# Performance work log

Hardware: AMD Instinct MI355X
Metric: run time of the kernel (lower is better)

Reference implementation:

```python
import jax, jax.numpy as jnp
import numpy as np

BCE_COEFF = 0.2
N_BOXES = 4194304


def setup_inputs() -> dict:
    key = jax.random.key(0)
    k1, k2, k3, k4, k5, k6, k7 = jax.random.split(key, 7)
    n = N_BOXES
    preds = jax.random.normal(k1, (n, 5), dtype=jnp.float32)
    # Build well-formed target boxes (x1<x2, y1<y2) with min size 0.1 in [0,1]
    x1 = jax.random.uniform(k2, (n,), dtype=jnp.float32) * 0.5
    y1 = jax.random.uniform(k3, (n,), dtype=jnp.float32) * 0.5
    w = 0.1 + 0.4 * jax.random.uniform(k4, (n,), dtype=jnp.float32)
    h = 0.1 + 0.4 * jax.random.uniform(k5, (n,), dtype=jnp.float32)
    lbl = jax.random.uniform(k6, (n,), dtype=jnp.float32)  # BCE targets in [0,1]
    target = jnp.stack([lbl, x1, y1, x1 + w, y1 + h], axis=1)
    return {"preds": preds, "target": target}


def _eiou_loss(p, t):
    # p, t: [n, 4] boxes (x1, y1, x2, y2); p already sigmoided
    pred_area = jnp.abs(p[:, 2] - p[:, 0]) * jnp.abs(p[:, 3] - p[:, 1])
    target_area = (t[:, 2] - t[:, 0]) * (t[:, 3] - t[:, 1])
    x_p1 = jnp.minimum(p[:, 2], p[:, 0])
    x_p2 = jnp.maximum(p[:, 2], p[:, 0])
    y_p1 = jnp.minimum(p[:, 1], p[:, 3])
    y_p2 = jnp.maximum(p[:, 1], p[:, 3])
    x1 = jnp.maximum(x_p1, t[:, 0])
    x2 = jnp.minimum(x_p2, t[:, 2])
    y1 = jnp.maximum(y_p1, t[:, 1])
    y2 = jnp.minimum(y_p2, t[:, 3])
    overlap = (x2 - x1) * (y2 - y1)
    overlap = jnp.where(overlap < 0, 0.0, overlap)  # faithful: clamp product only
    x1_c = jnp.minimum(x_p1, t[:, 0])
    x2_c = jnp.maximum(x_p2, t[:, 2])
    y1_c = jnp.minimum(y_p1, t[:, 1])
    y2_c = jnp.maximum(y_p2, t[:, 3])
    c_w = x2_c - x1_c
    c_h = y2_c - y1_c
    w = x_p2 - x_p1
    w_t = t[:, 2] - t[:, 0]
    h = y_p2 - y_p1
    h_t = t[:, 3] - t[:, 1]
    iou = overlap / (target_area + pred_area - overlap)
    cpx = (x_p2 + x_p1) * 0.5
    cpy = (y_p2 + y_p1) * 0.5
    ctx = (t[:, 2] + t[:, 0]) * 0.5
    cty = (t[:, 3] + t[:, 1]) * 0.5
    diag = c_w ** 2 + c_h ** 2
    center_part = ((cpx - ctx) ** 2 + (cpy - cty) ** 2) / diag
    width_part = (w - w_t) ** 2 / c_w ** 2
    height_part = (h - h_t) ** 2 / h_t ** 2  # faithful: h_t**2 denominator
    return 1.0 - (iou - (center_part + width_part + height_part))


def reference(preds, target):
    p_box = jax.nn.sigmoid(preds[:, 1:5])
    eiou = jnp.mean(_eiou_loss(p_box, target[:, 1:5]))
    # binary_cross_entropy_with_logits, mean reduction (numerically stable)
    x = preds[:, 0]
    y = target[:, 0]
    bce = jnp.mean(jnp.maximum(x, 0.0) - x * y + jnp.log1p(jnp.exp(-jnp.abs(x))))
    return BCE_COEFF * bce + eiou
```

## Files before the change

kernel.cpp:

```cpp
#include <hip/hip_runtime.h>

#define N_BOXES 4194304
#define BCE_COEFF 0.2f
#define BLOCK 256
#define WAVES 4
#define WCHUNK 128
#define F4_IN (WCHUNK * 5 / 4)
#define F4_TOT (F4_IN * 2)
#define NBLOCKS 1024
#define BOXES_PER_WAVE (N_BOXES / NBLOCKS / WAVES)
#define ROUNDS (BOXES_PER_WAVE / WCHUNK)

__device__ __forceinline__ void g2lds16(const float4* g, float4* l) {
    __builtin_amdgcn_global_load_lds(
        (const __attribute__((address_space(1))) void*)g,
        (__attribute__((address_space(3))) void*)l,
        16, 0, 0);
}

__global__ __launch_bounds__(BLOCK) void eiou_main(
        const float* __restrict__ preds,
        const float* __restrict__ target,
        float* __restrict__ slots) {
    __shared__ float4 sbuf[WAVES][2][F4_TOT];

    const int t    = threadIdx.x;
    const int lane = t & 63;
    const int w    = t >> 6;
    const float4* const p4 = reinterpret_cast<const float4*>(preds);
    const float4* const t4 = reinterpret_cast<const float4*>(target);

    const size_t wbase = (size_t)blockIdx.x * (N_BOXES / NBLOCKS * 5 / 4)
                       + (size_t)w * (BOXES_PER_WAVE * 5 / 4);

    auto stage = [&](int c, int b) {
        const size_t fb = wbase + (size_t)c * F4_IN;
#pragma unroll
        for (int k = 0; k < 5; ++k) {
            const int q = k * 64 + lane;
            const float4* src = (q < F4_IN) ? (p4 + fb + q)
                                            : (t4 + fb + (q - F4_IN));
            g2lds16(src, &sbuf[w][b][q]);
        }
    };

    stage(0, 0);
    float acc = 0.0f;

    for (int c = 0; c < ROUNDS; ++c) {
        const int b = c & 1;
        if (c + 1 < ROUNDS) {
            asm volatile("s_waitcnt lgkmcnt(0)" ::: "memory");
            stage(c + 1, b ^ 1);
            asm volatile("s_waitcnt vmcnt(5)" ::: "memory");
        } else {
            asm volatile("s_waitcnt vmcnt(0)" ::: "memory");
        }

        const float* __restrict__ s = reinterpret_cast<const float*>(&sbuf[w][b][0]);
#pragma unroll
        for (int j = 0; j < 2; ++j) {
            const int box = lane + j * 64;
            const float* __restrict__ P = s + box * 5;
            const float* __restrict__ T = s + WCHUNK * 5 + box * 5;

            const float x = P[0];
            const float y = T[0];
            const float p0 = __fdividef(1.0f, 1.0f + __expf(-P[1]));
            const float p1 = __fdividef(1.0f, 1.0f + __expf(-P[2]));
            const float p2 = __fdividef(1.0f, 1.0f + __expf(-P[3]));
            const float p3 = __fdividef(1.0f, 1.0f + __expf(-P[4]));
            const float t0 = T[1], t1 = T[2], t2 = T[3], t3 = T[4];

            const float pred_area   = fabsf(p2 - p0) * fabsf(p3 - p1);
            const float target_area = (t2 - t0) * (t3 - t1);

            const float xp1 = fminf(p2, p0), xp2 = fmaxf(p2, p0);
            const float yp1 = fminf(p1, p3), yp2 = fmaxf(p1, p3);

            const float x1 = fmaxf(xp1, t0), x2 = fminf(xp2, t2);
            const float y1 = fmaxf(yp1, t1), y2 = fminf(yp2, t3);

            float ov = (x2 - x1) * (y2 - y1);
            ov = (ov < 0.0f) ? 0.0f : ov;

            const float x1c = fminf(xp1, t0), x2c = fmaxf(xp2, t2);
            const float y1c = fminf(yp1, t1), y2c = fmaxf(yp2, t3);

            const float cw = x2c - x1c, ch = y2c - y1c;
            const float w2 = xp2 - xp1, wt = t2 - t0;
            const float h  = yp2 - yp1, ht = t3 - t1;

            const float iou = __fdividef(ov, target_area + pred_area - ov);

            const float cpx = (xp2 + xp1) * 0.5f, cpy = (yp2 + yp1) * 0.5f;
            const float ctx = (t2 + t0) * 0.5f,   cty = (t3 + t1) * 0.5f;
            const float diag = cw * cw + ch * ch;
            const float dx = cpx - ctx, dy = cpy - cty;

            const float center_part = __fdividef(dx * dx + dy * dy, diag);
            const float dwv = w2 - wt;
            const float width_part  = __fdividef(dwv * dwv, cw * cw);
            const float dhv = h - ht;
            const float height_part = __fdividef(dhv * dhv, ht * ht);

            const float eiou = 1.0f - (iou - (center_part + width_part + height_part));

            const float bce = fmaxf(x, 0.0f) - x * y
                            + __logf(1.0f + __expf(-fabsf(x)));

            acc += BCE_COEFF * bce + eiou;
        }
    }

#pragma unroll
    for (int off = 32; off > 0; off >>= 1)
        acc += __shfl_down(acc, off);

    __syncthreads();
    float* sf = reinterpret_cast<float*>(&sbuf[0][0][0]);
    if (lane == 0) sf[w] = acc;
    __syncthreads();
    if (t == 0) slots[blockIdx.x] = (sf[0] + sf[1]) + (sf[2] + sf[3]);
}

__global__ __launch_bounds__(256) void reduce_slots_kernel(
        const float* __restrict__ slots,
        float* __restrict__ out) {
    const float4 v4 = reinterpret_cast<const float4*>(slots)[threadIdx.x];
    float v = (v4.x + v4.y) + (v4.z + v4.w);
#pragma unroll
    for (int off = 32; off > 0; off >>= 1)
        v += __shfl_down(v, off);

    __shared__ float ws[4];
    const int lane = threadIdx.x & 63;
    const int wid  = threadIdx.x >> 6;
    if (lane == 0) ws[wid] = v;
    __syncthreads();
    if (threadIdx.x == 0)
        out[0] = ((ws[0] + ws[1]) + (ws[2] + ws[3])) * (1.0f / (float)N_BOXES);
}

extern "C" void kernel_launch(void* const* d_in, const int* in_sizes, int n_in,
                              void* d_out, int out_size, void* d_ws, size_t ws_size,
                              hipStream_t stream) {
    const float* preds  = (const float*)d_in[0];
    const float* target = (const float*)d_in[1];
    float* slots = (float*)d_ws;
    float* out   = (float*)d_out;

    eiou_main<<<NBLOCKS, BLOCK, 0, stream>>>(preds, target, slots);
    reduce_slots_kernel<<<1, 256, 0, stream>>>(slots, out);
}
```

Measured before the change: 34.19 us.

## Fuse final reduction into main kernel via per-block flags and merge width/height divides

Removes the second reduction kernel launch. Each block publishes its partial sum and sets a flag. Block 0 then spins on all flags, sums the partials and writes the output. The per-box math is also rearranged so the width and height terms share a single division over a common denominator. In exchange, block 0 busy-waits on the other blocks, which relies on the flags starting at zero and on every block becoming resident. The merged fraction can also change rounding slightly.

```diff
diff --git a/kernel.cpp b/kernel.cpp
--- a/kernel.cpp
+++ b/kernel.cpp
@@ -21,7 +21,9 @@
 __global__ __launch_bounds__(BLOCK) void eiou_main(
         const float* __restrict__ preds,
         const float* __restrict__ target,
-        float* __restrict__ slots) {
+        float* __restrict__ slots,
+        unsigned* __restrict__ flags,
+        float* __restrict__ out) {
     __shared__ float4 sbuf[WAVES][2][F4_TOT];
 
     const int t    = threadIdx.x;
@@ -72,11 +74,15 @@
             const float p3 = __fdividef(1.0f, 1.0f + __expf(-P[4]));
             const float t0 = T[1], t1 = T[2], t2 = T[3], t3 = T[4];
 
-            const float pred_area   = fabsf(p2 - p0) * fabsf(p3 - p1);
-            const float target_area = (t2 - t0) * (t3 - t1);
-
             const float xp1 = fminf(p2, p0), xp2 = fmaxf(p2, p0);
             const float yp1 = fminf(p1, p3), yp2 = fmaxf(p1, p3);
+
+            const float wv = xp2 - xp1;
+            const float h  = yp2 - yp1;
+            const float wt = t2 - t0;
+            const float ht = t3 - t1;
+            const float pred_area   = wv * h;
+            const float target_area = wt * ht;
 
             const float x1 = fmaxf(xp1, t0), x2 = fminf(xp2, t2);
             const float y1 = fmaxf(yp1, t1), y2 = fminf(yp2, t3);
@@ -88,23 +94,19 @@
             const float y1c = fminf(yp1, t1), y2c = fmaxf(yp2, t3);
 
             const float cw = x2c - x1c, ch = y2c - y1c;
-            const float w2 = xp2 - xp1, wt = t2 - t0;
-            const float h  = yp2 - yp1, ht = t3 - t1;
 
             const float iou = __fdividef(ov, target_area + pred_area - ov);
 
-            const float cpx = (xp2 + xp1) * 0.5f, cpy = (yp2 + yp1) * 0.5f;
-            const float ctx = (t2 + t0) * 0.5f,   cty = (t3 + t1) * 0.5f;
+            const float dx = 0.5f * ((xp1 + xp2) - (t0 + t2));
+            const float dy = 0.5f * ((yp1 + yp2) - (t1 + t3));
             const float diag = cw * cw + ch * ch;
-            const float dx = cpx - ctx, dy = cpy - cty;
+            const float center_part = __fdividef(dx * dx + dy * dy, diag);
 
-            const float center_part = __fdividef(dx * dx + dy * dy, diag);
-            const float dwv = w2 - wt;
-            const float width_part  = __fdividef(dwv * dwv, cw * cw);
-            const float dhv = h - ht;
-            const float height_part = __fdividef(dhv * dhv, ht * ht);
+            const float dwv = wv - wt, dhv = h - ht;
+            const float a = dwv * ht, bb = dhv * cw, d = cw * ht;
+            const float wh_part = __fdividef(a * a + bb * bb, d * d);
 
-            const float eiou = 1.0f - (iou - (center_part + width_part + height_part));
+            const float eiou = 1.0f - (iou - (center_part + wh_part));
 
             const float bce = fmaxf(x, 0.0f) - x * y
                             + __logf(1.0f + __expf(-fabsf(x)));
@@ -121,25 +123,33 @@
     float* sf = reinterpret_cast<float*>(&sbuf[0][0][0]);
     if (lane == 0) sf[w] = acc;
     __syncthreads();
-    if (t == 0) slots[blockIdx.x] = (sf[0] + sf[1]) + (sf[2] + sf[3]);
-}
 
-__global__ __launch_bounds__(256) void reduce_slots_kernel(
-        const float* __restrict__ slots,
-        float* __restrict__ out) {
-    const float4 v4 = reinterpret_cast<const float4*>(slots)[threadIdx.x];
-    float v = (v4.x + v4.y) + (v4.z + v4.w);
+    if (t == 0) {
+        const float bs = (sf[0] + sf[1]) + (sf[2] + sf[3]);
+        atomicExch(&slots[blockIdx.x], bs);
+        __threadfence();
+        atomicExch(&flags[blockIdx.x], 1u);
+    }
+
+    if (blockIdx.x == 0) {
+        float v = 0.0f;
 #pragma unroll
-    for (int off = 32; off > 0; off >>= 1)
-        v += __shfl_down(v, off);
+        for (int k = 0; k < NBLOCKS / BLOCK; ++k) {
+            const int i = t + k * BLOCK;
+            while (atomicCAS(&flags[i], 1u, 0u) != 1u)
+                __builtin_amdgcn_s_sleep(1);
+            v += atomicAdd(&slots[i], 0.0f);
+        }
+#pragma unroll
+        for (int off = 32; off > 0; off >>= 1)
+            v += __shfl_down(v, off);
 
-    __shared__ float ws[4];
-    const int lane = threadIdx.x & 63;
-    const int wid  = threadIdx.x >> 6;
-    if (lane == 0) ws[wid] = v;
-    __syncthreads();
-    if (threadIdx.x == 0)
-        out[0] = ((ws[0] + ws[1]) + (ws[2] + ws[3])) * (1.0f / (float)N_BOXES);
+        __syncthreads();
+        if (lane == 0) sf[w] = v;
+        __syncthreads();
+        if (t == 0)
+            out[0] = ((sf[0] + sf[1]) + (sf[2] + sf[3])) * (1.0f / (float)N_BOXES);
+    }
 }
 
 extern "C" void kernel_launch(void* const* d_in, const int* in_sizes, int n_in,
@@ -147,9 +157,9 @@
                               hipStream_t stream) {
     const float* preds  = (const float*)d_in[0];
     const float* target = (const float*)d_in[1];
-    float* slots = (float*)d_ws;
-    float* out   = (float*)d_out;
+    float*    slots = (float*)d_ws;
+    unsigned* flags = (unsigned*)((char*)d_ws + NBLOCKS * sizeof(float));
+    float*    out   = (float*)d_out;
 
-    eiou_main<<<NBLOCKS, BLOCK, 0, stream>>>(preds, target, slots);
-    reduce_slots_kernel<<<1, 256, 0, stream>>>(slots, out);
+    eiou_main<<<NBLOCKS, BLOCK, 0, stream>>>(preds, target, slots, flags, out);
 }
```

New measurement: 58.62 us. 71.5% more time.

## Halve per-wave chunk, double blocks, merge width/height divisions into one

Applied to the files above, without the earlier changes.

Shrinks the per-wave staging chunk from 128 to 64 boxes and doubles the grid to 2048 blocks, with a launch-bounds occupancy hint of 8 blocks per CU, so more waves are resident to hide memory latency. Each lane now handles one box per round, and the async LDS staging issues 3 guarded loads instead of 5, with the wait count adjusted to match. The width and height terms are combined over a common denominator so one fast division replaces two, and pred_area reuses the already computed width and height. The final reduction kernel grows to 512 threads to cover the larger slot array. The trade-off is more rounds per wave, each with a synchronisation wait, and slightly different floating-point rounding.

```diff
diff --git a/kernel.cpp b/kernel.cpp
--- a/kernel.cpp
+++ b/kernel.cpp
@@ -4,10 +4,10 @@
 #define BCE_COEFF 0.2f
 #define BLOCK 256
 #define WAVES 4
-#define WCHUNK 128
+#define WCHUNK 64
 #define F4_IN (WCHUNK * 5 / 4)
 #define F4_TOT (F4_IN * 2)
-#define NBLOCKS 1024
+#define NBLOCKS 2048
 #define BOXES_PER_WAVE (N_BOXES / NBLOCKS / WAVES)
 #define ROUNDS (BOXES_PER_WAVE / WCHUNK)
 
@@ -18,7 +18,7 @@
         16, 0, 0);
 }
 
-__global__ __launch_bounds__(BLOCK) void eiou_main(
+__global__ __launch_bounds__(BLOCK, 8) void eiou_main(
         const float* __restrict__ preds,
         const float* __restrict__ target,
         float* __restrict__ slots) {
@@ -36,11 +36,13 @@
     auto stage = [&](int c, int b) {
         const size_t fb = wbase + (size_t)c * F4_IN;
 #pragma unroll
-        for (int k = 0; k < 5; ++k) {
+        for (int k = 0; k < 3; ++k) {
             const int q = k * 64 + lane;
-            const float4* src = (q < F4_IN) ? (p4 + fb + q)
-                                            : (t4 + fb + (q - F4_IN));
-            g2lds16(src, &sbuf[w][b][q]);
+            if (q < F4_TOT) {
+                const float4* src = (q < F4_IN) ? (p4 + fb + q)
+                                                : (t4 + fb + (q - F4_IN));
+                g2lds16(src, &sbuf[w][b][q]);
+            }
         }
     };
 
@@ -52,65 +54,61 @@
         if (c + 1 < ROUNDS) {
             asm volatile("s_waitcnt lgkmcnt(0)" ::: "memory");
             stage(c + 1, b ^ 1);
-            asm volatile("s_waitcnt vmcnt(5)" ::: "memory");
+            asm volatile("s_waitcnt vmcnt(3)" ::: "memory");
         } else {
             asm volatile("s_waitcnt vmcnt(0)" ::: "memory");
         }
 
         const float* __restrict__ s = reinterpret_cast<const float*>(&sbuf[w][b][0]);
-#pragma unroll
-        for (int j = 0; j < 2; ++j) {
-            const int box = lane + j * 64;
-            const float* __restrict__ P = s + box * 5;
-            const float* __restrict__ T = s + WCHUNK * 5 + box * 5;
+        const float* __restrict__ P = s + lane * 5;
+        const float* __restrict__ T = s + WCHUNK * 5 + lane * 5;
 
-            const float x = P[0];
-            const float y = T[0];
-            const float p0 = __fdividef(1.0f, 1.0f + __expf(-P[1]));
-            const float p1 = __fdividef(1.0f, 1.0f + __expf(-P[2]));
-            const float p2 = __fdividef(1.0f, 1.0f + __expf(-P[3]));
-            const float p3 = __fdividef(1.0f, 1.0f + __expf(-P[4]));
-            const float t0 = T[1], t1 = T[2], t2 = T[3], t3 = T[4];
+        const float x = P[0];
+        const float y = T[0];
+        const float p0 = __fdividef(1.0f, 1.0f + __expf(-P[1]));
+        const float p1 = __fdividef(1.0f, 1.0f + __expf(-P[2]));
+        const float p2 = __fdividef(1.0f, 1.0f + __expf(-P[3]));
+        const float p3 = __fdividef(1.0f, 1.0f + __expf(-P[4]));
+        const float t0 = T[1], t1 = T[2], t2 = T[3], t3 = T[4];
 
-            const float pred_area   = fabsf(p2 - p0) * fabsf(p3 - p1);
-            const float target_area = (t2 - t0) * (t3 - t1);
+        const float xp1 = fminf(p2, p0), xp2 = fmaxf(p2, p0);
+        const float yp1 = fminf(p1, p3), yp2 = fmaxf(p1, p3);
 
-            const float xp1 = fminf(p2, p0), xp2 = fmaxf(p2, p0);
-            const float yp1 = fminf(p1, p3), yp2 = fmaxf(p1, p3);
+        const float wv = xp2 - xp1;
+        const float h  = yp2 - yp1;
+        const float wt = t2 - t0;
+        const float ht = t3 - t1;
+        const float pred_area   = wv * h;
+        const float target_area = wt * ht;
 
-            const float x1 = fmaxf(xp1, t0), x2 = fminf(xp2, t2);
-            const float y1 = fmaxf(yp1, t1), y2 = fminf(yp2, t3);
+        const float x1 = fmaxf(xp1, t0), x2 = fminf(xp2, t2);
+        const float y1 = fmaxf(yp1, t1), y2 = fminf(yp2, t3);
 
-            float ov = (x2 - x1) * (y2 - y1);
-            ov = (ov < 0.0f) ? 0.0f : ov;
+        float ov = (x2 - x1) * (y2 - y1);
+        ov = (ov < 0.0f) ? 0.0f : ov;
 
-            const float x1c = fminf(xp1, t0), x2c = fmaxf(xp2, t2);
-            const float y1c = fminf(yp1, t1), y2c = fmaxf(yp2, t3);
+        const float x1c = fminf(xp1, t0), x2c = fmaxf(xp2, t2);
+        const float y1c = fminf(yp1, t1), y2c = fmaxf(yp2, t3);
 
-            const float cw = x2c - x1c, ch = y2c - y1c;
-            const float w2 = xp2 - xp1, wt = t2 - t0;
-            const float h  = yp2 - yp1, ht = t3 - t1;
+        const float cw = x2c - x1c, ch = y2c - y1c;
 
-            const float iou = __fdividef(ov, target_area + pred_area - ov);
+        const float iou = __fdividef(ov, target_area + pred_area - ov);
 
-            const float cpx = (xp2 + xp1) * 0.5f, cpy = (yp2 + yp1) * 0.5f;
-            const float ctx = (t2 + t0) * 0.5f,   cty = (t3 + t1) * 0.5f;
-            const float diag = cw * cw + ch * ch;
-            const float dx = cpx - ctx, dy = cpy - cty;
+        const float dx = 0.5f * ((xp1 + xp2) - (t0 + t2));
+        const float dy = 0.5f * ((yp1 + yp2) - (t1 + t3));
+        const float diag = cw * cw + ch * ch;
+        const float center_part = __fdividef(dx * dx + dy * dy, diag);
 
-            const float center_part = __fdividef(dx * dx + dy * dy, diag);
-            const float dwv = w2 - wt;
-            const float width_part  = __fdividef(dwv * dwv, cw * cw);
-            const float dhv = h - ht;
-            const float height_part = __fdividef(dhv * dhv, ht * ht);
+        const float dwv = wv - wt, dhv = h - ht;
+        const float a = dwv * ht, bb = dhv * cw, d = cw * ht;
+        const float wh_part = __fdividef(a * a + bb * bb, d * d);
 
-            const float eiou = 1.0f - (iou - (center_part + width_part + height_part));
+        const float eiou = 1.0f - (iou - (center_part + wh_part));
 
-            const float bce = fmaxf(x, 0.0f) - x * y
-                            + __logf(1.0f + __expf(-fabsf(x)));
+        const float bce = fmaxf(x, 0.0f) - x * y
+                        + __logf(1.0f + __expf(-fabsf(x)));
 
-            acc += BCE_COEFF * bce + eiou;
-        }
+        acc += BCE_COEFF * bce + eiou;
     }
 
 #pragma unroll
@@ -124,7 +122,7 @@
     if (t == 0) slots[blockIdx.x] = (sf[0] + sf[1]) + (sf[2] + sf[3]);
 }
 
-__global__ __launch_bounds__(256) void reduce_slots_kernel(
+__global__ __launch_bounds__(512) void reduce_slots_kernel(
         const float* __restrict__ slots,
         float* __restrict__ out) {
     const float4 v4 = reinterpret_cast<const float4*>(slots)[threadIdx.x];
@@ -133,13 +131,17 @@
     for (int off = 32; off > 0; off >>= 1)
         v += __shfl_down(v, off);
 
-    __shared__ float ws[4];
+    __shared__ float ws[8];
     const int lane = threadIdx.x & 63;
     const int wid  = threadIdx.x >> 6;
     if (lane == 0) ws[wid] = v;
     __syncthreads();
-    if (threadIdx.x == 0)
-        out[0] = ((ws[0] + ws[1]) + (ws[2] + ws[3])) * (1.0f / (float)N_BOXES);
+    if (threadIdx.x == 0) {
+        float s = 0.0f;
+#pragma unroll
+        for (int i = 0; i < 8; ++i) s += ws[i];
+        out[0] = s * (1.0f / (float)N_BOXES);
+    }
 }
 
 extern "C" void kernel_launch(void* const* d_in, const int* in_sizes, int n_in,
@@ -151,5 +153,5 @@
     float* out   = (float*)d_out;
 
     eiou_main<<<NBLOCKS, BLOCK, 0, stream>>>(preds, target, slots);
-    reduce_slots_kernel<<<1, 256, 0, stream>>>(slots, out);
+    reduce_slots_kernel<<<1, 512, 0, stream>>>(slots, out);
 }
```

After: 32.94 us. 3.7% less time.
